# Performance work log

Hardware: AMD Instinct MI355X
Metric: run time of the kernel (lower is better)

The kernel has to match this reference:

```python
import jax, jax.numpy as jnp
import numpy as np

B, FRAMES, IMG, PATCH = 2, 4, 224, 16
D_MODEL, D_INNER, D_STATE, DT_RANK, DEPTH, D_CONV = 256, 512, 16, 16, 12, 4
NPATCH = (IMG // PATCH) ** 2  # 196


def setup_inputs() -> dict:
    keys = iter(jax.random.split(jax.random.key(0), 80))

    def n(shape, s=0.02):
        return jax.random.normal(next(keys), shape, dtype=jnp.float32) * s

    A_init = jnp.broadcast_to(jnp.log(jnp.arange(1, D_STATE + 1, dtype=jnp.float32)), (DEPTH, D_INNER, D_STATE))
    inp = {
        'x': jax.random.normal(next(keys), (B, 3, FRAMES, IMG, IMG), dtype=jnp.float32),
        'patch_w': n((D_MODEL, 3, 1, PATCH, PATCH)),
        'patch_b': jnp.zeros((D_MODEL,), jnp.float32),
        'pos_embed': n((1, NPATCH, D_MODEL)),
        'temp_pos': n((1, FRAMES, D_MODEL)),
        'in_proj_w': n((DEPTH, 2 * D_INNER, D_MODEL), D_MODEL ** -0.5),
        'convf_w': n((DEPTH, D_INNER, D_CONV), 0.3),
        'convf_b': jnp.zeros((DEPTH, D_INNER), jnp.float32),
        'xprojf_w': n((DEPTH, DT_RANK + 2 * D_STATE, D_INNER), D_INNER ** -0.5),
        'dtf_w': n((DEPTH, D_INNER, DT_RANK), DT_RANK ** -0.5),
        'dtf_b': jnp.full((DEPTH, D_INNER), -4.6, jnp.float32) + n((DEPTH, D_INNER), 0.1),
        'A_logf': A_init,
        'Dsf': jnp.ones((DEPTH, D_INNER), jnp.float32),
        'convb_w': n((DEPTH, D_INNER, D_CONV), 0.3),
        'convb_b': jnp.zeros((DEPTH, D_INNER), jnp.float32),
        'xprojb_w': n((DEPTH, DT_RANK + 2 * D_STATE, D_INNER), D_INNER ** -0.5),
        'dtb_w': n((DEPTH, D_INNER, DT_RANK), DT_RANK ** -0.5),
        'dtb_b': jnp.full((DEPTH, D_INNER), -4.6, jnp.float32) + n((DEPTH, D_INNER), 0.1),
        'A_logb': A_init,
        'Dsb': jnp.ones((DEPTH, D_INNER), jnp.float32),
        'out_proj_w': n((DEPTH, D_MODEL, D_INNER), D_INNER ** -0.5),
        'norm_w': jnp.ones((DEPTH, D_MODEL), jnp.float32),
        'normf_w': jnp.ones((D_MODEL,), jnp.float32),
        'bbox_w1': n((D_MODEL, D_MODEL), D_MODEL ** -0.5),
        'bbox_b1': jnp.zeros((D_MODEL,), jnp.float32),
        'bbox_w2': n((3, D_MODEL), D_MODEL ** -0.5),
        'bbox_b2': jnp.zeros((3,), jnp.float32),
        'pix_w1': n((4, D_MODEL, D_MODEL), D_MODEL ** -0.5),
        'pix_b1': jnp.zeros((4, D_MODEL), jnp.float32),
        'pix_w2': n((4, 2, D_MODEL), D_MODEL ** -0.5),
        'pix_b2': jnp.zeros((4, 2), jnp.float32),
    }
    return inp


def rmsnorm(x, w, eps=1e-5):
    x = x.astype(jnp.float32)
    return x * jax.lax.rsqrt(jnp.mean(x * x, axis=-1, keepdims=True) + eps) * w


def ssm_scan(u, dt, A, Bm, Cm):
    # u, dt: [B,L,di]; Bm, Cm: [B,L,st]; A: [di,st]
    def step(h, inp):
        dt_t, B_t, C_t, u_t = inp  # [B,di],[B,st],[B,st],[B,di]
        h = jnp.exp(dt_t[..., None] * A) * h + (dt_t * u_t)[..., None] * B_t[:, None, :]
        return h, jnp.einsum('bds,bs->bd', h, C_t)
    h0 = jnp.zeros((u.shape[0], u.shape[2], A.shape[1]), u.dtype)
    xs = (dt.swapaxes(0, 1), Bm.swapaxes(0, 1), Cm.swapaxes(0, 1), u.swapaxes(0, 1))
    _, ys = jax.lax.scan(step, h0, xs)
    return ys.swapaxes(0, 1)  # [B,L,di]


def mamba_dir(x, z, cw, cb, xpw, dtw, dtb, A_log, Ds):
    L = x.shape[1]
    xp = jnp.pad(x, ((0, 0), (D_CONV - 1, 0), (0, 0)))  # causal depthwise conv
    xc = cb + sum(xp[:, k:k + L, :] * cw[:, k] for k in range(D_CONV))
    xs = jax.nn.silu(xc)
    dbl = xs @ xpw.T  # [B,L,dt_rank+2*st]
    dt = jax.nn.softplus(dbl[..., :DT_RANK] @ dtw.T + dtb)
    Bm = dbl[..., DT_RANK:DT_RANK + D_STATE]
    Cm = dbl[..., DT_RANK + D_STATE:]
    y = ssm_scan(xs, dt, -jnp.exp(A_log), Bm, Cm) + Ds * xs
    return y * jax.nn.silu(z)


def _forward(x, patch_w, patch_b, pos_embed, temp_pos, in_proj_w, convf_w, convf_b, xprojf_w, dtf_w, dtf_b, A_logf, Dsf, convb_w, convb_b, xprojb_w, dtb_w, dtb_b, A_logb, Dsb, out_proj_w, norm_w, normf_w, bbox_w1, bbox_b1, bbox_w2, bbox_b2, pix_w1, pix_b1, pix_w2, pix_b2):
    feat = jax.lax.conv_general_dilated(x, patch_w, (1, PATCH, PATCH), 'VALID', dimension_numbers=('NCDHW', 'OIDHW', 'NCDHW'))
    feat = feat + patch_b[None, :, None, None, None]
    b, c, t, h, w = feat.shape
    np_ = h * w
    tok = feat.transpose(0, 2, 3, 4, 1).reshape(b * t, np_, c) + pos_embed
    tok = tok.reshape(b, t, np_, c).transpose(0, 2, 1, 3).reshape(b * np_, t, c) + temp_pos
    tok = tok.reshape(b, np_, t, c).transpose(0, 2, 1, 3).reshape(b, t * np_, c)
    hidden, residual = tok, None
    for i in range(DEPTH):
        residual = hidden if residual is None else hidden + residual  # fused add+norm (prenorm)
        hidden = rmsnorm(residual, norm_w[i])
        xz = hidden @ in_proj_w[i].T
        xi, zi = jnp.split(xz, 2, axis=-1)
        yf = mamba_dir(xi, zi, convf_w[i], convf_b[i], xprojf_w[i], dtf_w[i], dtf_b[i], A_logf[i], Dsf[i])
        yb = mamba_dir(xi[:, ::-1], zi[:, ::-1], convb_w[i], convb_b[i], xprojb_w[i], dtb_w[i], dtb_b[i], A_logb[i], Dsb[i])[:, ::-1]
        hidden = (yf + yb) @ out_proj_w[i].T
    residual = hidden + residual
    hidden = rmsnorm(residual, normf_w)
    fus = hidden[:, :5, :]  # [B,5,hidden_dim] fusion_output for DETR head
    bbox = jax.nn.relu(fus[:, 0] @ bbox_w1.T + bbox_b1) @ bbox_w2.T + bbox_b2  # [B,3]
    pix = jnp.stack([jax.nn.sigmoid(jax.nn.relu(fus[:, i + 1] @ pix_w1[i].T + pix_b1[i]) @ pix_w2[i].T + pix_b2[i]) for i in range(4)], axis=1)  # [B,4,2]
    return jnp.concatenate([bbox, pix.reshape(bbox.shape[0], 8)], axis=-1)  # [B,11]


def reference(x, patch_w, patch_b, pos_embed, temp_pos, in_proj_w, convf_w, convf_b, xprojf_w, dtf_w, dtf_b, A_logf, Dsf, convb_w, convb_b, xprojb_w, dtb_w, dtb_b, A_logb, Dsb, out_proj_w, norm_w, normf_w, bbox_w1, bbox_b1, bbox_w2, bbox_b2, pix_w1, pix_b1, pix_w2, pix_b2):
    return _forward(x, patch_w, patch_b, pos_embed, temp_pos, in_proj_w, convf_w, convf_b, xprojf_w, dtf_w, dtf_b, A_logf, Dsf, convb_w, convb_b, xprojb_w, dtb_w, dtb_b, A_logb, Dsb, out_proj_w, norm_w, normf_w, bbox_w1, bbox_b1, bbox_w2, bbox_b2, pix_w1, pix_b1, pix_w2, pix_b2)
```

## Files before the change

### kernel.cpp

```cpp
#include <hip/hip_runtime.h>
#include <hip/hip_bf16.h>
#include <cmath>

#define BB 2
#define TT 4
#define NPATCH 196
#define LL 784
#define CC 256
#define DI 512
#define NSTATE 16
#define DEPTH 12
#define NCHUNK 49
#define CLEN 16
#define CTAU 8

typedef short short8 __attribute__((ext_vector_type(8)));
typedef float f32x4 __attribute__((ext_vector_type(4)));

__device__ __forceinline__ float sigmoidf_(float x){ return 1.f/(1.f+__expf(-x)); }
__device__ __forceinline__ float siluf_(float x){ return x/(1.f+__expf(-x)); }
__device__ __forceinline__ float softplusf_(float x){ return x > 20.f ? x : log1pf(__expf(x)); }
__device__ __forceinline__ unsigned short f2bf(float f){
  union { float f; unsigned int u; } v; v.f = f;
  unsigned int u = v.u;
  return (unsigned short)((u + 0x7FFFu + ((u>>16)&1u)) >> 16);
}
__device__ __forceinline__ float bf2f(unsigned short u){
  union { unsigned int i; float f; } v; v.i = ((unsigned int)u)<<16; return v.f;
}

#define PREP_NA 3072
#define PREP_NB 1536
#define PREP_NC 192
#define PREP_ND 1536
#define PREP_NE 1536
#define PREP_NF 784
#define PREP_NG 4704
__global__ void k_prep_all(
    const float* __restrict__ in_proj, unsigned short* __restrict__ WinB,
    const float* __restrict__ out_proj, unsigned short* __restrict__ WoutB,
    const float* __restrict__ patch_w, unsigned short* __restrict__ WpB,
    const float* __restrict__ xpf, const float* __restrict__ xpb, unsigned short* __restrict__ Wxp,
    const float* __restrict__ dtwf, const float* __restrict__ dtwb, unsigned short* __restrict__ Wdt,
    const float* __restrict__ pb, const float* __restrict__ pos, const float* __restrict__ tpos,
    float* __restrict__ PB,
    const float* __restrict__ x, unsigned short* __restrict__ XCol)
{
  int blk = blockIdx.x;
  if (blk < PREP_NA + PREP_NB + PREP_NC) {
    const float* src; unsigned short* dst; int i;
    if (blk < PREP_NA)                  { src = in_proj;  dst = WinB;  i = blk*256 + threadIdx.x; }
    else if (blk < PREP_NA + PREP_NB)   { src = out_proj; dst = WoutB; i = (blk-PREP_NA)*256 + threadIdx.x; }
    else                                { src = patch_w;  dst = WpB;   i = (blk-PREP_NA-PREP_NB)*256 + threadIdx.x; }
    float4 v = *(const float4*)(src + (size_t)i*4);
    unsigned short o[4] = { f2bf(v.x), f2bf(v.y), f2bf(v.z), f2bf(v.w) };
    *(uint2*)(dst + (size_t)i*4) = *(uint2*)o;
    return;
  }
  blk -= PREP_NA + PREP_NB + PREP_NC;
  if (blk < PREP_ND) {
    int r = blk & 63; int ld = blk >> 6;
    int layer = ld >> 1, dir = ld & 1;
    const float* src = dir ? xpb : xpf;
    for (int kk = threadIdx.x; kk < 512; kk += 256) {
      float v = (r < 48) ? src[((size_t)layer*48 + r)*512 + kk] : 0.f;
      Wxp[((size_t)blk)*512 + kk] = f2bf(v);
    }
    return;
  }
  blk -= PREP_ND;
  if (blk < PREP_NE) {
    int idx = blk*256 + threadIdx.x;
    int col = idx & 31; int rest = idx >> 5;
    int d = rest & 511; int ld = rest >> 9;
    int layer = ld >> 1, dir = ld & 1;
    const float* src = dir ? dtwb : dtwf;
    float v = (col < 16) ? src[((size_t)layer*512 + d)*16 + col] : 0.f;
    Wdt[idx] = f2bf(v);
    return;
  }
  blk -= PREP_NE;
  if (blk < PREP_NF) {
    int tp = blk;
    int t = tp / NPATCH, p = tp - t*NPATCH;
    int c = threadIdx.x;
    PB[(size_t)tp*CC + c] = pb[c] + pos[(size_t)p*CC + c] + tpos[(size_t)t*CC + c];
    return;
  }
  blk -= PREP_NF;
  {
    int ci = blk / (BB*LL);
    int row = blk - ci*(BB*LL);
    int b = row / LL, rem = row - b*LL;
    int t = rem / NPATCH, p = rem - t*NPATCH;
    int ph = p / 14, pc = p - ph*14;
    int ii = threadIdx.x >> 4, jj = threadIdx.x & 15;
    float v = x[(((size_t)(b*3+ci)*TT + t)*224 + (ph*16+ii))*224 + (pc*16+jj)];
    XCol[(size_t)row*768 + ci*256 + threadIdx.x] = f2bf(v);
  }
}

__global__ __launch_bounds__(256) void k_gemm_mfma(
    const unsigned short* __restrict__ Ab, const unsigned short* __restrict__ Ab2,
    const unsigned short* __restrict__ Wb,
    float* __restrict__ Out, unsigned short* __restrict__ Outb,
    const float* __restrict__ bias, int M, int Nn, int K)
{
  __shared__ short As[64][40];
  __shared__ short Bs[64][40];
  int bm = blockIdx.x*64, bn = blockIdx.y*64;
  int tid = threadIdx.x;
  int wave = tid>>6, lane = tid&63;
  int wm = (wave>>1)*32, wn = (wave&1)*32;
  int quad = lane>>4, l16 = lane&15;
  f32x4 acc[2][2];
  #pragma unroll
  for (int i=0;i<2;i++)
    #pragma unroll
    for (int j=0;j<2;j++){ acc[i][j][0]=0.f; acc[i][j][1]=0.f; acc[i][j][2]=0.f; acc[i][j][3]=0.f; }
  int sr = tid>>2, sc = (tid&3)<<3;
  int gr = bm + sr;
  for (int k0 = 0; k0 < K; k0 += 32) {
    short8 av = {0,0,0,0,0,0,0,0};
    if (gr < M) {
      av = *(const short8*)(Ab + (size_t)gr*K + k0 + sc);
      if (Ab2) {
        short8 a2v = *(const short8*)(Ab2 + (size_t)gr*K + k0 + sc);
        #pragma unroll
        for (int j=0;j<8;j++)
          av[j] = (short)f2bf(bf2f((unsigned short)av[j]) + bf2f((unsigned short)a2v[j]));
      }
    }
    *(short8*)&As[sr][sc] = av;
    short8 bv = *(const short8*)(Wb + (size_t)(bn+sr)*K + k0 + sc);
    *(short8*)&Bs[sr][sc] = bv;
    __syncthreads();
    short8 a0 = *(const short8*)&As[wm    +l16][quad<<3];
    short8 a1 = *(const short8*)&As[wm+16+l16][quad<<3];
    short8 b0 = *(const short8*)&Bs[wn    +l16][quad<<3];
    short8 b1 = *(const short8*)&Bs[wn+16+l16][quad<<3];
    acc[0][0] = __builtin_amdgcn_mfma_f32_16x16x32_bf16(a0,b0,acc[0][0],0,0,0);
    acc[0][1] = __builtin_amdgcn_mfma_f32_16x16x32_bf16(a0,b1,acc[0][1],0,0,0);
    acc[1][0] = __builtin_amdgcn_mfma_f32_16x16x32_bf16(a1,b0,acc[1][0],0,0,0);
    acc[1][1] = __builtin_amdgcn_mfma_f32_16x16x32_bf16(a1,b1,acc[1][1],0,0,0);
    __syncthreads();
  }
  #pragma unroll
  for (int i=0;i<2;i++){
    #pragma unroll
    for (int r=0;r<4;r++){
      int row = bm + wm + i*16 + quad*4 + r;
      if (row < M) {
        #pragma unroll
        for (int j=0;j<2;j++){
          int col = bn + wn + j*16 + l16;
          float vv = acc[i][j][r];
          if (bias) vv += bias[(size_t)(row % LL)*Nn + col];
          if (Outb) Outb[(size_t)row*Nn + col] = f2bf(vv);
          else      Out [(size_t)row*Nn + col] = vv;
        }
      }
    }
  }
}

__global__ __launch_bounds__(256) void k_gemm_xp(
    const unsigned short* __restrict__ XSb, const unsigned short* __restrict__ Wxp,
    float* __restrict__ DBL, unsigned short* __restrict__ DBLb)
{
  __shared__ short As[64][40];
  __shared__ short Bs[64][40];
  int z = blockIdx.z;
  int bm = blockIdx.x*64;
  const unsigned short* A = XSb + (size_t)z*2*LL*DI;
  const unsigned short* W = Wxp + (size_t)z*64*DI;
  int tid = threadIdx.x;
  int wave = tid>>6, lane = tid&63;
  int wm = (wave>>1)*32, wn = (wave&1)*32;
  int quad = lane>>4, l16 = lane&15;
  f32x4 acc[2][2];
  #pragma unroll
  for (int i=0;i<2;i++)
    #pragma unroll
    for (int j=0;j<2;j++){ acc[i][j][0]=0.f; acc[i][j][1]=0.f; acc[i][j][2]=0.f; acc[i][j][3]=0.f; }
  int sr = tid>>2, sc = (tid&3)<<3;
  int gr = bm + sr;
  for (int k0 = 0; k0 < DI; k0 += 32) {
    short8 av = {0,0,0,0,0,0,0,0};
    if (gr < 2*LL) av = *(const short8*)(A + (size_t)gr*DI + k0 + sc);
    *(short8*)&As[sr][sc] = av;
    *(short8*)&Bs[sr][sc] = *(const short8*)(W + (size_t)sr*DI + k0 + sc);
    __syncthreads();
    short8 a0 = *(const short8*)&As[wm    +l16][quad<<3];
    short8 a1 = *(const short8*)&As[wm+16+l16][quad<<3];
    short8 b0 = *(const short8*)&Bs[wn    +l16][quad<<3];
    short8 b1 = *(const short8*)&Bs[wn+16+l16][quad<<3];
    acc[0][0] = __builtin_amdgcn_mfma_f32_16x16x32_bf16(a0,b0,acc[0][0],0,0,0);
    acc[0][1] = __builtin_amdgcn_mfma_f32_16x16x32_bf16(a0,b1,acc[0][1],0,0,0);
    acc[1][0] = __builtin_amdgcn_mfma_f32_16x16x32_bf16(a1,b0,acc[1][0],0,0,0);
    acc[1][1] = __builtin_amdgcn_mfma_f32_16x16x32_bf16(a1,b1,acc[1][1],0,0,0);
    __syncthreads();
  }
  #pragma unroll
  for (int i=0;i<2;i++){
    #pragma unroll
    for (int r=0;r<4;r++){
      int row = bm + wm + i*16 + quad*4 + r;
      if (row < 2*LL) {
        size_t grow = (size_t)z*2*LL + row;
        #pragma unroll
        for (int j=0;j<2;j++){
          int col = wn + j*16 + l16;
          float vv = acc[i][j][r];
          DBL[grow*64 + col] = vv;
          if (col < 32) DBLb[grow*32 + col] = (col < 16) ? f2bf(vv) : (unsigned short)0;
        }
      }
    }
  }
}

__global__ __launch_bounds__(256) void k_gemm_dt(
    const unsigned short* __restrict__ DBLb, const unsigned short* __restrict__ Wdt,
    const float* __restrict__ dtbf, const float* __restrict__ dtbb,
    float* __restrict__ DTs)
{
  __shared__ short As[64][40];
  __shared__ short Bs[64][40];
  int z = blockIdx.z;
  int bm = blockIdx.x*64, bn = blockIdx.y*64;
  const unsigned short* A = DBLb + (size_t)z*2*LL*32;
  const unsigned short* W = Wdt + (size_t)z*DI*32;
  const float* dtb = z ? dtbb : dtbf;
  int tid = threadIdx.x;
  int wave = tid>>6, lane = tid&63;
  int wm = (wave>>1)*32, wn = (wave&1)*32;
  int quad = lane>>4, l16 = lane&15;
  f32x4 acc[2][2];
  #pragma unroll
  for (int i=0;i<2;i++)
    #pragma unroll
    for (int j=0;j<2;j++){ acc[i][j][0]=0.f; acc[i][j][1]=0.f; acc[i][j][2]=0.f; acc[i][j][3]=0.f; }
  int sr = tid>>2, sc = (tid&3)<<3;
  int gr = bm + sr;
  {
    short8 av = {0,0,0,0,0,0,0,0};
    if (gr < 2*LL) av = *(const short8*)(A + (size_t)gr*32 + sc);
    *(short8*)&As[sr][sc] = av;
    *(short8*)&Bs[sr][sc] = *(const short8*)(W + (size_t)(bn+sr)*32 + sc);
    __syncthreads();
    short8 a0 = *(const short8*)&As[wm    +l16][quad<<3];
    short8 a1 = *(const short8*)&As[wm+16+l16][quad<<3];
    short8 b0 = *(const short8*)&Bs[wn    +l16][quad<<3];
    short8 b1 = *(const short8*)&Bs[wn+16+l16][quad<<3];
    acc[0][0] = __builtin_amdgcn_mfma_f32_16x16x32_bf16(a0,b0,acc[0][0],0,0,0);
    acc[0][1] = __builtin_amdgcn_mfma_f32_16x16x32_bf16(a0,b1,acc[0][1],0,0,0);
    acc[1][0] = __builtin_amdgcn_mfma_f32_16x16x32_bf16(a1,b0,acc[1][0],0,0,0);
    acc[1][1] = __builtin_amdgcn_mfma_f32_16x16x32_bf16(a1,b1,acc[1][1],0,0,0);
  }
  #pragma unroll
  for (int i=0;i<2;i++){
    #pragma unroll
    for (int r=0;r<4;r++){
      int row = bm + wm + i*16 + quad*4 + r;
      if (row < 2*LL) {
        size_t grow = (size_t)z*2*LL + row;
        #pragma unroll
        for (int j=0;j<2;j++){
          int col = bn + wn + j*16 + l16;
          DTs[grow*DI + col] = softplusf_(acc[i][j][r] + dtb[col]);
        }
      }
    }
  }
}

__global__ void k_conv_silu(const unsigned short* __restrict__ XZb,
    const float* __restrict__ cwf, const float* __restrict__ cbf,
    const float* __restrict__ cwb, const float* __restrict__ cbb,
    unsigned short* __restrict__ XSb)
{
  int dir = blockIdx.z;
  int blk = blockIdx.x;
  int b = blk / (LL/CTAU), tq = blk - b*(LL/CTAU);
  int t0 = tq * CTAU;
  const float* cw = dir ? cwb : cwf;
  const float* cb = dir ? cbb : cbf;
  int d = threadIdx.x;
  float4 w4 = *(const float4*)(cw + (size_t)d*4);
  float bia = cb[d];
  const unsigned short* xz = XZb + (size_t)b*LL*1024 + d;
  float x0 = 0.f, x1 = 0.f, x2 = 0.f;
  {
    int tt = t0-3; if (tt >= 0) x0 = bf2f(xz[(size_t)(dir ? (LL-1-tt) : tt)*1024]);
    tt = t0-2;     if (tt >= 0) x1 = bf2f(xz[(size_t)(dir ? (LL-1-tt) : tt)*1024]);
    tt = t0-1;     if (tt >= 0) x2 = bf2f(xz[(size_t)(dir ? (LL-1-tt) : tt)*1024]);
  }
  size_t rowbase = ((size_t)(dir*BB + b)*LL + t0)*DI + d;
  #pragma unroll
  for (int i = 0; i < CTAU; ++i) {
    int tt = t0 + i;
    int torig = dir ? (LL-1-tt) : tt;
    float xin = bf2f(xz[(size_t)torig*1024]);
    float acc = bia;
    acc = fmaf(x0, w4.x, acc);
    acc = fmaf(x1, w4.y, acc);
    acc = fmaf(x2, w4.z, acc);
    acc = fmaf(xin, w4.w, acc);
    XSb[rowbase + (size_t)i*DI] = f2bf(siluf_(acc));
    x0 = x1; x1 = x2; x2 = xin;
  }
}

__global__ void k_res_rms(const float* __restrict__ Hin, float* __restrict__ R,
                          unsigned short* __restrict__ Nout, const float* __restrict__ w, int first)
{
  int row = blockIdx.x, c = threadIdx.x;
  size_t idx = (size_t)row*CC + c;
  float h = Hin[idx];
  float r = first ? h : (h + R[idx]);
  R[idx] = r;
  float v = r*r;
  #pragma unroll
  for (int m=1;m<64;m<<=1) v += __shfl_xor(v,m);
  __shared__ float sred[4];
  if ((c & 63)==0) sred[c>>6]=v;
  __syncthreads();
  float tot = sred[0]+sred[1]+sred[2]+sred[3];
  float sc = rsqrtf(tot*(1.f/CC) + 1e-5f);
  Nout[idx] = f2bf(r*sc*w[c]);
}

__global__ void k_scan1(const unsigned short* __restrict__ XSb, const float* __restrict__ DBL,
                        const float* __restrict__ DTs,
                        const float* __restrict__ Alf, const float* __restrict__ Alb,
                        float* __restrict__ Pb, float* __restrict__ Hcb)
{
  int chunk = blockIdx.x;
  int d = blockIdx.y*256 + threadIdx.x;
  int dirb = blockIdx.z;
  int dir = dirb >> 1;
  const float* Al = dir ? Alb : Alf;
  float a2[NSTATE];
  {
    const float4* ar = (const float4*)(Al + (size_t)d*NSTATE);
    #pragma unroll
    for (int q=0;q<4;q++){
      float4 v = ar[q];
      a2[q*4+0] = -__expf(v.x)*1.44269504f;
      a2[q*4+1] = -__expf(v.y)*1.44269504f;
      a2[q*4+2] = -__expf(v.z)*1.44269504f;
      a2[q*4+3] = -__expf(v.w)*1.44269504f;
    }
  }
  __shared__ float Bl[CLEN][NSTATE];
  {
    int t = threadIdx.x >> 4, s = threadIdx.x & 15;
    size_t row = ((size_t)dirb*LL + chunk*CLEN + t)*64;
    Bl[t][s] = DBL[row + 16 + s];
  }
  __syncthreads();
  size_t base = (size_t)dirb*LL*DI;
  const unsigned short* xs = XSb + base + (size_t)chunk*CLEN*DI + d;
  const float* dtp = DTs + base + (size_t)chunk*CLEN*DI + d;
  float P[NSTATE], h[NSTATE];
  #pragma unroll
  for (int s=0;s<NSTATE;s++){ P[s]=1.f; h[s]=0.f; }
  for (int i = 0; i < CLEN; ++i) {
    float dt = dtp[(size_t)i*DI];
    float u  = bf2f(xs[(size_t)i*DI]);
    float du = dt*u;
    #pragma unroll
    for (int s=0;s<NSTATE;s++){
      float e = exp2f(dt*a2[s]);
      P[s] *= e;
      h[s] = fmaf(e, h[s], du*Bl[i][s]);
    }
  }
  size_t ob = ((size_t)dirb*NCHUNK + chunk)*NSTATE*DI + d;
  #pragma unroll
  for (int s=0;s<NSTATE;s++){
    Pb [ob + (size_t)s*DI] = P[s];
    Hcb[ob + (size_t)s*DI] = h[s];
  }
}

__global__ void k_scan2(const float* __restrict__ Pb, float* __restrict__ Hcb)
{
  int i = blockIdx.x*256 + threadIdx.x;
  int dirb = blockIdx.y;
  float h = 0.f;
  for (int c = 0; c < NCHUNK; ++c) {
    size_t idx = ((size_t)dirb*NCHUNK + c)*NSTATE*DI + i;
    float p = Pb[idx], hl = Hcb[idx];
    Hcb[idx] = h;
    h = fmaf(p, h, hl);
  }
}

__global__ void k_scan3(const unsigned short* __restrict__ XSb, const float* __restrict__ DBL,
                        const float* __restrict__ DTs, const unsigned short* __restrict__ XZb,
                        const float* __restrict__ Alf, const float* __restrict__ Alb,
                        const float* __restrict__ Dsfp, const float* __restrict__ Dsbp,
                        const float* __restrict__ Hcb, unsigned short* __restrict__ Yb)
{
  int chunk = blockIdx.x;
  int d = blockIdx.y*256 + threadIdx.x;
  int dirb = blockIdx.z;
  int dir = dirb >> 1, b = dirb & 1;
  const float* Al = dir ? Alb : Alf;
  float a2[NSTATE];
  {
    const float4* ar = (const float4*)(Al + (size_t)d*NSTATE);
    #pragma unroll
    for (int q=0;q<4;q++){
      float4 v = ar[q];
      a2[q*4+0] = -__expf(v.x)*1.44269504f;
      a2[q*4+1] = -__expf(v.y)*1.44269504f;
      a2[q*4+2] = -__expf(v.z)*1.44269504f;
      a2[q*4+3] = -__expf(v.w)*1.44269504f;
    }
  }
  __shared__ float BCl[CLEN][32];
  {
    for (int idx = threadIdx.x; idx < CLEN*32; idx += 256) {
      int t = idx >> 5, j = idx & 31;
      size_t row = ((size_t)dirb*LL + chunk*CLEN + t)*64;
      BCl[t][j] = DBL[row + 16 + j];
    }
  }
  __syncthreads();
  float h[NSTATE];
  size_t ob = ((size_t)dirb*NCHUNK + chunk)*NSTATE*DI + d;
  #pragma unroll
  for (int s=0;s<NSTATE;s++) h[s] = Hcb[ob + (size_t)s*DI];
  float Dsv = (dir ? Dsbp : Dsfp)[d];
  size_t base = (size_t)dirb*LL*DI;
  const unsigned short* xs = XSb + base + (size_t)chunk*CLEN*DI + d;
  const float* dtp = DTs + base + (size_t)chunk*CLEN*DI + d;
  const unsigned short* zpb = XZb + (size_t)b*LL*1024 + 512 + d;
  unsigned short* y = Yb + base + d;
  for (int i = 0; i < CLEN; ++i) {
    int tau = chunk*CLEN + i;
    float dt = dtp[(size_t)i*DI];
    float u  = bf2f(xs[(size_t)i*DI]);
    float du = dt*u;
    float yacc = 0.f;
    #pragma unroll
    for (int s=0;s<NSTATE;s++){
      float e = exp2f(dt*a2[s]);
      h[s] = fmaf(e, h[s], du*BCl[i][s]);
      yacc = fmaf(h[s], BCl[i][16+s], yacc);
    }
    int torig = dir ? (LL-1-tau) : tau;
    float zv = bf2f(zpb[(size_t)torig*1024]);
    y[(size_t)torig*DI] = f2bf((yacc + Dsv*u) * siluf_(zv));
  }
}

__global__ void k_head(const float* __restrict__ H, const float* __restrict__ R,
                       const float* __restrict__ nw,
                       const float* __restrict__ bw1, const float* __restrict__ bb1,
                       const float* __restrict__ bw2, const float* __restrict__ bb2,
                       const float* __restrict__ pw1, const float* __restrict__ pb1,
                       const float* __restrict__ pw2, const float* __restrict__ pb2,
                       float* __restrict__ out)
{
  int b = blockIdx.x / 5, j = blockIdx.x % 5;
  int c = threadIdx.x;
  __shared__ float fus[CC], h1[CC];
  __shared__ float sred[4];
  size_t idx = ((size_t)b*LL + j)*CC + c;
  float r = H[idx] + R[idx];
  float v = r*r;
  #pragma unroll
  for (int m=1;m<64;m<<=1) v += __shfl_xor(v,m);
  if ((c&63)==0) sred[c>>6]=v;
  __syncthreads();
  float tot = sred[0]+sred[1]+sred[2]+sred[3];
  fus[c] = r * rsqrtf(tot*(1.f/CC)+1e-5f) * nw[c];
  __syncthreads();
  const float* W1 = (j==0) ? bw1 : (pw1 + (size_t)(j-1)*CC*CC);
  const float* B1 = (j==0) ? bb1 : (pb1 + (j-1)*CC);
  float a = B1[c];
  for (int k=0;k<CC;k++) a = fmaf(fus[k], W1[(size_t)c*CC+k], a);
  h1[c] = fmaxf(a, 0.f);
  __syncthreads();
  if (j==0) {
    if (c < 3) {
      float o = bb2[c];
      for (int k=0;k<CC;k++) o = fmaf(h1[k], bw2[c*CC+k], o);
      out[b*11 + c] = o;
    }
  } else {
    if (c < 2) {
      const float* W2 = pw2 + (size_t)((j-1)*2 + c)*CC;
      float o = pb2[(j-1)*2 + c];
      for (int k=0;k<CC;k++) o = fmaf(h1[k], W2[k], o);
      out[b*11 + 3 + (j-1)*2 + c] = sigmoidf_(o);
    }
  }
}

extern "C" void kernel_launch(void* const* d_in, const int* in_sizes, int n_in,
                              void* d_out, int out_size, void* d_ws, size_t ws_size,
                              hipStream_t stream)
{
  const float* x        = (const float*)d_in[0];
  const float* patch_w  = (const float*)d_in[1];
  const float* patch_b  = (const float*)d_in[2];
  const float* pos      = (const float*)d_in[3];
  const float* tpos     = (const float*)d_in[4];
  const float* in_proj  = (const float*)d_in[5];
  const float* convf_w  = (const float*)d_in[6];
  const float* convf_b  = (const float*)d_in[7];
  const float* xprojf_w = (const float*)d_in[8];
  const float* dtf_w    = (const float*)d_in[9];
  const float* dtf_b    = (const float*)d_in[10];
  const float* A_logf   = (const float*)d_in[11];
  const float* Dsf      = (const float*)d_in[12];
  const float* convb_w  = (const float*)d_in[13];
  const float* convb_b  = (const float*)d_in[14];
  const float* xprojb_w = (const float*)d_in[15];
  const float* dtb_w    = (const float*)d_in[16];
  const float* dtb_b    = (const float*)d_in[17];
  const float* A_logb   = (const float*)d_in[18];
  const float* Dsb      = (const float*)d_in[19];
  const float* out_proj = (const float*)d_in[20];
  const float* norm_w   = (const float*)d_in[21];
  const float* normf_w  = (const float*)d_in[22];
  const float* bbox_w1  = (const float*)d_in[23];
  const float* bbox_b1  = (const float*)d_in[24];
  const float* bbox_w2  = (const float*)d_in[25];
  const float* bbox_b2  = (const float*)d_in[26];
  const float* pix_w1   = (const float*)d_in[27];
  const float* pix_b1   = (const float*)d_in[28];
  const float* pix_w2   = (const float*)d_in[29];
  const float* pix_b2   = (const float*)d_in[30];
  float* out = (float*)d_out;

  float* ws = (float*)d_ws;
  const size_t nTok = (size_t)BB*LL;
  float* H   = ws;                 ws += nTok*CC;
  float* R   = ws;                 ws += nTok*CC;
  float* DBL = ws;                 ws += 2*nTok*64;
  float* DTs = ws;                 ws += 2*nTok*DI;
  float* Pb  = ws;                 ws += (size_t)4*NCHUNK*NSTATE*DI;
  float* Hcb = ws;                 ws += (size_t)4*NCHUNK*NSTATE*DI;
  float* PB  = ws;                 ws += (size_t)LL*CC;
  unsigned short* WinB  = (unsigned short*)ws;  ws += (size_t)DEPTH*1024*CC/2;
  unsigned short* WoutB = (unsigned short*)ws;  ws += (size_t)DEPTH*CC*DI/2;
  unsigned short* WpB   = (unsigned short*)ws;  ws += (size_t)CC*768/2;
  unsigned short* XCol  = (unsigned short*)ws;  ws += nTok*768/2;
  unsigned short* NrmB  = (unsigned short*)ws;  ws += nTok*CC/2;
  unsigned short* XZb   = (unsigned short*)ws;  ws += nTok*1024/2;
  unsigned short* XSb   = (unsigned short*)ws;  ws += 2*nTok*DI/2;
  unsigned short* DBLb  = (unsigned short*)ws;  ws += 2*nTok*32/2;
  unsigned short* Yb    = (unsigned short*)ws;  ws += 2*nTok*DI/2;
  unsigned short* Wxp   = (unsigned short*)ws;  ws += (size_t)DEPTH*2*64*DI/2;
  unsigned short* Wdt   = (unsigned short*)ws;  ws += (size_t)DEPTH*2*DI*32/2;
  (void)ws_size; (void)in_sizes; (void)n_in; (void)out_size;

  {
    const unsigned prepBlocks = PREP_NA + PREP_NB + PREP_NC + PREP_ND + PREP_NE + PREP_NF + PREP_NG;
    k_prep_all<<<dim3(prepBlocks), 256, 0, stream>>>(
        in_proj, WinB, out_proj, WoutB, patch_w, WpB,
        xprojf_w, xprojb_w, Wxp, dtf_w, dtb_w, Wdt,
        patch_b, pos, tpos, PB, x, XCol);
  }
  k_gemm_mfma<<<dim3(25, 4), 256, 0, stream>>>(XCol, nullptr, WpB, H, nullptr, PB,
                                               (int)nTok, CC, 768);

  for (int i = 0; i < DEPTH; ++i) {
    k_res_rms<<<dim3((unsigned)nTok), 256, 0, stream>>>(H, R, NrmB, norm_w + i*CC, i==0 ? 1 : 0);
    k_gemm_mfma<<<dim3(25, 16), 256, 0, stream>>>(NrmB, nullptr,
        WinB + (size_t)i*1024*CC, nullptr, XZb, nullptr, (int)nTok, 1024, CC);
    k_conv_silu<<<dim3(BB*LL/CTAU, 1, 2), DI, 0, stream>>>(XZb,
        convf_w + (size_t)i*DI*4, convf_b + (size_t)i*DI,
        convb_w + (size_t)i*DI*4, convb_b + (size_t)i*DI, XSb);
    k_gemm_xp<<<dim3(25, 1, 2), 256, 0, stream>>>(XSb,
        Wxp + (size_t)i*2*64*DI, DBL, DBLb);
    k_gemm_dt<<<dim3(25, 8, 2), 256, 0, stream>>>(DBLb,
        Wdt + (size_t)i*2*DI*32, dtf_b + (size_t)i*DI, dtb_b + (size_t)i*DI, DTs);
    k_scan1<<<dim3(NCHUNK, 2, 4), 256, 0, stream>>>(XSb, DBL, DTs,
        A_logf + (size_t)i*DI*NSTATE, A_logb + (size_t)i*DI*NSTATE, Pb, Hcb);
    k_scan2<<<dim3(32, 4), 256, 0, stream>>>(Pb, Hcb);
    k_scan3<<<dim3(NCHUNK, 2, 4), 256, 0, stream>>>(XSb, DBL, DTs, XZb,
        A_logf + (size_t)i*DI*NSTATE, A_logb + (size_t)i*DI*NSTATE,
        Dsf + (size_t)i*DI, Dsb + (size_t)i*DI, Hcb, Yb);
    k_gemm_mfma<<<dim3(25, 4), 256, 0, stream>>>(Yb, Yb + nTok*DI,
        WoutB + (size_t)i*CC*DI, H, nullptr, nullptr, (int)nTok, CC, DI);
  }
  k_head<<<dim3(10), 256, 0, stream>>>(H, R, normf_w, bbox_w1, bbox_b1, bbox_w2, bbox_b2,
                                       pix_w1, pix_b1, pix_w2, pix_b2, out);
}
```

Before: 1.256 ms.

## Fuse dt projection into scan kernels and fold chunk-prefix pass into scan3

```diff
diff --git a/kernel.cpp b/kernel.cpp
--- a/kernel.cpp
+++ b/kernel.cpp
@@ -33,7 +33,6 @@
 #define PREP_NB 1536
 #define PREP_NC 192
 #define PREP_ND 1536
-#define PREP_NE 1536
 #define PREP_NF 784
 #define PREP_NG 4704
 __global__ void k_prep_all(
@@ -41,7 +40,6 @@
     const float* __restrict__ out_proj, unsigned short* __restrict__ WoutB,
     const float* __restrict__ patch_w, unsigned short* __restrict__ WpB,
     const float* __restrict__ xpf, const float* __restrict__ xpb, unsigned short* __restrict__ Wxp,
-    const float* __restrict__ dtwf, const float* __restrict__ dtwb, unsigned short* __restrict__ Wdt,
     const float* __restrict__ pb, const float* __restrict__ pos, const float* __restrict__ tpos,
     float* __restrict__ PB,
     const float* __restrict__ x, unsigned short* __restrict__ XCol)
@@ -69,17 +67,6 @@
     return;
   }
   blk -= PREP_ND;
-  if (blk < PREP_NE) {
-    int idx = blk*256 + threadIdx.x;
-    int col = idx & 31; int rest = idx >> 5;
-    int d = rest & 511; int ld = rest >> 9;
-    int layer = ld >> 1, dir = ld & 1;
-    const float* src = dir ? dtwb : dtwf;
-    float v = (col < 16) ? src[((size_t)layer*512 + d)*16 + col] : 0.f;
-    Wdt[idx] = f2bf(v);
-    return;
-  }
-  blk -= PREP_NE;
   if (blk < PREP_NF) {
     int tp = blk;
     int t = tp / NPATCH, p = tp - t*NPATCH;
@@ -166,7 +153,7 @@
 
 __global__ __launch_bounds__(256) void k_gemm_xp(
     const unsigned short* __restrict__ XSb, const unsigned short* __restrict__ Wxp,
-    float* __restrict__ DBL, unsigned short* __restrict__ DBLb)
+    float* __restrict__ DBL)
 {
   __shared__ short As[64][40];
   __shared__ short Bs[64][40];
@@ -211,64 +198,7 @@
         #pragma unroll
         for (int j=0;j<2;j++){
           int col = wn + j*16 + l16;
-          float vv = acc[i][j][r];
-          DBL[grow*64 + col] = vv;
-          if (col < 32) DBLb[grow*32 + col] = (col < 16) ? f2bf(vv) : (unsigned short)0;
-        }
-      }
-    }
-  }
-}
-
-__global__ __launch_bounds__(256) void k_gemm_dt(
-    const unsigned short* __restrict__ DBLb, const unsigned short* __restrict__ Wdt,
-    const float* __restrict__ dtbf, const float* __restrict__ dtbb,
-    float* __restrict__ DTs)
-{
-  __shared__ short As[64][40];
-  __shared__ short Bs[64][40];
-  int z = blockIdx.z;
-  int bm = blockIdx.x*64, bn = blockIdx.y*64;
-  const unsigned short* A = DBLb + (size_t)z*2*LL*32;
-  const unsigned short* W = Wdt + (size_t)z*DI*32;
-  const float* dtb = z ? dtbb : dtbf;
-  int tid = threadIdx.x;
-  int wave = tid>>6, lane = tid&63;
-  int wm = (wave>>1)*32, wn = (wave&1)*32;
-  int quad = lane>>4, l16 = lane&15;
-  f32x4 acc[2][2];
-  #pragma unroll
-  for (int i=0;i<2;i++)
-    #pragma unroll
-    for (int j=0;j<2;j++){ acc[i][j][0]=0.f; acc[i][j][1]=0.f; acc[i][j][2]=0.f; acc[i][j][3]=0.f; }
-  int sr = tid>>2, sc = (tid&3)<<3;
-  int gr = bm + sr;
-  {
-    short8 av = {0,0,0,0,0,0,0,0};
-    if (gr < 2*LL) av = *(const short8*)(A + (size_t)gr*32 + sc);
-    *(short8*)&As[sr][sc] = av;
-    *(short8*)&Bs[sr][sc] = *(const short8*)(W + (size_t)(bn+sr)*32 + sc);
-    __syncthreads();
-    short8 a0 = *(const short8*)&As[wm    +l16][quad<<3];
-    short8 a1 = *(const short8*)&As[wm+16+l16][quad<<3];
-    short8 b0 = *(const short8*)&Bs[wn    +l16][quad<<3];
-    short8 b1 = *(const short8*)&Bs[wn+16+l16][quad<<3];
-    acc[0][0] = __builtin_amdgcn_mfma_f32_16x16x32_bf16(a0,b0,acc[0][0],0,0,0);
-    acc[0][1] = __builtin_amdgcn_mfma_f32_16x16x32_bf16(a0,b1,acc[0][1],0,0,0);
-    acc[1][0] = __builtin_amdgcn_mfma_f32_16x16x32_bf16(a1,b0,acc[1][0],0,0,0);
-    acc[1][1] = __builtin_amdgcn_mfma_f32_16x16x32_bf16(a1,b1,acc[1][1],0,0,0);
-  }
-  #pragma unroll
-  for (int i=0;i<2;i++){
-    #pragma unroll
-    for (int r=0;r<4;r++){
-      int row = bm + wm + i*16 + quad*4 + r;
-      if (row < 2*LL) {
-        size_t grow = (size_t)z*2*LL + row;
-        #pragma unroll
-        for (int j=0;j<2;j++){
-          int col = bn + wn + j*16 + l16;
-          DTs[grow*DI + col] = softplusf_(acc[i][j][r] + dtb[col]);
+          DBL[grow*64 + col] = acc[i][j][r];
         }
       }
     }
@@ -332,7 +262,8 @@
 }
 
 __global__ void k_scan1(const unsigned short* __restrict__ XSb, const float* __restrict__ DBL,
-                        const float* __restrict__ DTs,
+                        const float* __restrict__ dtwf, const float* __restrict__ dtwb,
+                        const float* __restrict__ dtbf, const float* __restrict__ dtbb,
                         const float* __restrict__ Alf, const float* __restrict__ Alb,
                         float* __restrict__ Pb, float* __restrict__ Hcb)
 {
@@ -341,9 +272,12 @@
   int dirb = blockIdx.z;
   int dir = dirb >> 1;
   const float* Al = dir ? Alb : Alf;
-  float a2[NSTATE];
+  const float* dtw = dir ? dtwb : dtwf;
+  float dtbv = (dir ? dtbb : dtbf)[d];
+  float a2[NSTATE], wd[NSTATE];
   {
     const float4* ar = (const float4*)(Al + (size_t)d*NSTATE);
+    const float4* wr = (const float4*)(dtw + (size_t)d*NSTATE);
     #pragma unroll
     for (int q=0;q<4;q++){
       float4 v = ar[q];
@@ -351,23 +285,28 @@
       a2[q*4+1] = -__expf(v.y)*1.44269504f;
       a2[q*4+2] = -__expf(v.z)*1.44269504f;
       a2[q*4+3] = -__expf(v.w)*1.44269504f;
-    }
-  }
-  __shared__ float Bl[CLEN][NSTATE];
+      float4 w = wr[q];
+      wd[q*4+0] = w.x; wd[q*4+1] = w.y; wd[q*4+2] = w.z; wd[q*4+3] = w.w;
+    }
+  }
+  __shared__ float Dl[CLEN][NSTATE], Bl[CLEN][NSTATE];
   {
     int t = threadIdx.x >> 4, s = threadIdx.x & 15;
     size_t row = ((size_t)dirb*LL + chunk*CLEN + t)*64;
+    Dl[t][s] = DBL[row + s];
     Bl[t][s] = DBL[row + 16 + s];
   }
   __syncthreads();
   size_t base = (size_t)dirb*LL*DI;
   const unsigned short* xs = XSb + base + (size_t)chunk*CLEN*DI + d;
-  const float* dtp = DTs + base + (size_t)chunk*CLEN*DI + d;
   float P[NSTATE], h[NSTATE];
   #pragma unroll
   for (int s=0;s<NSTATE;s++){ P[s]=1.f; h[s]=0.f; }
   for (int i = 0; i < CLEN; ++i) {
-    float dt = dtp[(size_t)i*DI];
+    float dtv = dtbv;
+    #pragma unroll
+    for (int r=0;r<NSTATE;r++) dtv = fmaf(Dl[i][r], wd[r], dtv);
+    float dt = softplusf_(dtv);
     float u  = bf2f(xs[(size_t)i*DI]);
     float du = dt*u;
     #pragma unroll
@@ -385,33 +324,26 @@
   }
 }
 
-__global__ void k_scan2(const float* __restrict__ Pb, float* __restrict__ Hcb)
-{
-  int i = blockIdx.x*256 + threadIdx.x;
-  int dirb = blockIdx.y;
-  float h = 0.f;
-  for (int c = 0; c < NCHUNK; ++c) {
-    size_t idx = ((size_t)dirb*NCHUNK + c)*NSTATE*DI + i;
-    float p = Pb[idx], hl = Hcb[idx];
-    Hcb[idx] = h;
-    h = fmaf(p, h, hl);
-  }
-}
-
 __global__ void k_scan3(const unsigned short* __restrict__ XSb, const float* __restrict__ DBL,
-                        const float* __restrict__ DTs, const unsigned short* __restrict__ XZb,
+                        const unsigned short* __restrict__ XZb,
+                        const float* __restrict__ dtwf, const float* __restrict__ dtwb,
+                        const float* __restrict__ dtbf, const float* __restrict__ dtbb,
                         const float* __restrict__ Alf, const float* __restrict__ Alb,
                         const float* __restrict__ Dsfp, const float* __restrict__ Dsbp,
-                        const float* __restrict__ Hcb, unsigned short* __restrict__ Yb)
+                        const float* __restrict__ Pb, const float* __restrict__ Hcb,
+                        unsigned short* __restrict__ Yb)
 {
   int chunk = blockIdx.x;
   int d = blockIdx.y*256 + threadIdx.x;
   int dirb = blockIdx.z;
   int dir = dirb >> 1, b = dirb & 1;
   const float* Al = dir ? Alb : Alf;
-  float a2[NSTATE];
+  const float* dtw = dir ? dtwb : dtwf;
+  float dtbv = (dir ? dtbb : dtbf)[d];
+  float a2[NSTATE], wd[NSTATE];
   {
     const float4* ar = (const float4*)(Al + (size_t)d*NSTATE);
+    const float4* wr = (const float4*)(dtw + (size_t)d*NSTATE);
     #pragma unroll
     for (int q=0;q<4;q++){
       float4 v = ar[q];
@@ -419,30 +351,43 @@
       a2[q*4+1] = -__expf(v.y)*1.44269504f;
       a2[q*4+2] = -__expf(v.z)*1.44269504f;
       a2[q*4+3] = -__expf(v.w)*1.44269504f;
-    }
-  }
+      float4 w = wr[q];
+      wd[q*4+0] = w.x; wd[q*4+1] = w.y; wd[q*4+2] = w.z; wd[q*4+3] = w.w;
+    }
+  }
+  __shared__ float Dl[CLEN][NSTATE];
   __shared__ float BCl[CLEN][32];
   {
-    for (int idx = threadIdx.x; idx < CLEN*32; idx += 256) {
-      int t = idx >> 5, j = idx & 31;
-      size_t row = ((size_t)dirb*LL + chunk*CLEN + t)*64;
-      BCl[t][j] = DBL[row + 16 + j];
-    }
+    int t = threadIdx.x >> 4, s = threadIdx.x & 15;
+    size_t row = ((size_t)dirb*LL + chunk*CLEN + t)*64;
+    Dl[t][s] = DBL[row + s];
+    BCl[t][s] = DBL[row + 16 + s];
+    BCl[t][16+s] = DBL[row + 32 + s];
   }
   __syncthreads();
   float h[NSTATE];
-  size_t ob = ((size_t)dirb*NCHUNK + chunk)*NSTATE*DI + d;
-  #pragma unroll
-  for (int s=0;s<NSTATE;s++) h[s] = Hcb[ob + (size_t)s*DI];
+  #pragma unroll
+  for (int s=0;s<NSTATE;s++) h[s] = 0.f;
+  for (int cc = 0; cc < chunk; ++cc) {
+    size_t ib = ((size_t)dirb*NCHUNK + cc)*NSTATE*DI + d;
+    #pragma unroll
+    for (int s=0;s<NSTATE;s++){
+      float p  = Pb [ib + (size_t)s*DI];
+      float hl = Hcb[ib + (size_t)s*DI];
+      h[s] = fmaf(p, h[s], hl);
+    }
+  }
   float Dsv = (dir ? Dsbp : Dsfp)[d];
   size_t base = (size_t)dirb*LL*DI;
   const unsigned short* xs = XSb + base + (size_t)chunk*CLEN*DI + d;
-  const float* dtp = DTs + base + (size_t)chunk*CLEN*DI + d;
   const unsigned short* zpb = XZb + (size_t)b*LL*1024 + 512 + d;
   unsigned short* y = Yb + base + d;
   for (int i = 0; i < CLEN; ++i) {
     int tau = chunk*CLEN + i;
-    float dt = dtp[(size_t)i*DI];
+    float dtv = dtbv;
+    #pragma unroll
+    for (int r=0;r<NSTATE;r++) dtv = fmaf(Dl[i][r], wd[r], dtv);
+    float dt = softplusf_(dtv);
     float u  = bf2f(xs[(size_t)i*DI]);
     float du = dt*u;
     float yacc = 0.f;
@@ -544,7 +489,6 @@
   float* H   = ws;                 ws += nTok*CC;
   float* R   = ws;                 ws += nTok*CC;
   float* DBL = ws;                 ws += 2*nTok*64;
-  float* DTs = ws;                 ws += 2*nTok*DI;
   float* Pb  = ws;                 ws += (size_t)4*NCHUNK*NSTATE*DI;
   float* Hcb = ws;                 ws += (size_t)4*NCHUNK*NSTATE*DI;
   float* PB  = ws;                 ws += (size_t)LL*CC;
@@ -555,17 +499,15 @@
   unsigned short* NrmB  = (unsigned short*)ws;  ws += nTok*CC/2;
   unsigned short* XZb   = (unsigned short*)ws;  ws += nTok*1024/2;
   unsigned short* XSb   = (unsigned short*)ws;  ws += 2*nTok*DI/2;
-  unsigned short* DBLb  = (unsigned short*)ws;  ws += 2*nTok*32/2;
   unsigned short* Yb    = (unsigned short*)ws;  ws += 2*nTok*DI/2;
   unsigned short* Wxp   = (unsigned short*)ws;  ws += (size_t)DEPTH*2*64*DI/2;
-  unsigned short* Wdt   = (unsigned short*)ws;  ws += (size_t)DEPTH*2*DI*32/2;
   (void)ws_size; (void)in_sizes; (void)n_in; (void)out_size;
 
   {
-    const unsigned prepBlocks = PREP_NA + PREP_NB + PREP_NC + PREP_ND + PREP_NE + PREP_NF + PREP_NG;
+    const unsigned prepBlocks = PREP_NA + PREP_NB + PREP_NC + PREP_ND + PREP_NF + PREP_NG;
     k_prep_all<<<dim3(prepBlocks), 256, 0, stream>>>(
         in_proj, WinB, out_proj, WoutB, patch_w, WpB,
-        xprojf_w, xprojb_w, Wxp, dtf_w, dtb_w, Wdt,
+        xprojf_w, xprojb_w, Wxp,
         patch_b, pos, tpos, PB, x, XCol);
   }
   k_gemm_mfma<<<dim3(25, 4), 256, 0, stream>>>(XCol, nullptr, WpB, H, nullptr, PB,
@@ -579,15 +521,16 @@
         convf_w + (size_t)i*DI*4, convf_b + (size_t)i*DI,
         convb_w + (size_t)i*DI*4, convb_b + (size_t)i*DI, XSb);
     k_gemm_xp<<<dim3(25, 1, 2), 256, 0, stream>>>(XSb,
-        Wxp + (size_t)i*2*64*DI, DBL, DBLb);
-    k_gemm_dt<<<dim3(25, 8, 2), 256, 0, stream>>>(DBLb,
-        Wdt + (size_t)i*2*DI*32, dtf_b + (size_t)i*DI, dtb_b + (size_t)i*DI, DTs);
-    k_scan1<<<dim3(NCHUNK, 2, 4), 256, 0, stream>>>(XSb, DBL, DTs,
+        Wxp + (size_t)i*2*64*DI, DBL);
+    k_scan1<<<dim3(NCHUNK, 2, 4), 256, 0, stream>>>(XSb, DBL,
+        dtf_w + (size_t)i*DI*16, dtb_w + (size_t)i*DI*16,
+        dtf_b + (size_t)i*DI, dtb_b + (size_t)i*DI,
         A_logf + (size_t)i*DI*NSTATE, A_logb + (size_t)i*DI*NSTATE, Pb, Hcb);
-    k_scan2<<<dim3(32, 4), 256, 0, stream>>>(Pb, Hcb);
-    k_scan3<<<dim3(NCHUNK, 2, 4), 256, 0, stream>>>(XSb, DBL, DTs, XZb,
+    k_scan3<<<dim3(NCHUNK, 2, 4), 256, 0, stream>>>(XSb, DBL, XZb,
+        dtf_w + (size_t)i*DI*16, dtb_w + (size_t)i*DI*16,
+        dtf_b + (size_t)i*DI, dtb_b + (size_t)i*DI,
         A_logf + (size_t)i*DI*NSTATE, A_logb + (size_t)i*DI*NSTATE,
-        Dsf + (size_t)i*DI, Dsb + (size_t)i*DI, Hcb, Yb);
+        Dsf + (size_t)i*DI, Dsb + (size_t)i*DI, Pb, Hcb, Yb);
     k_gemm_mfma<<<dim3(25, 4), 256, 0, stream>>>(Yb, Yb + nTok*DI,
         WoutB + (size_t)i*CC*DI, H, nullptr, nullptr, (int)nTok, CC, DI);
   }
```

Result: slower. 1.485 ms (+18.2%).
